# Kernel optimization log

Measured on AMD Instinct MI355X. Metric: run time of the kernel, lower is better.

## Reference

```python
import jax, jax.numpy as jnp
import numpy as np

C = 128
EPS = 1e-5


def _ln(x, g, b):
    m = jnp.mean(x, axis=-1, keepdims=True)
    v = jnp.mean((x - m) ** 2, axis=-1, keepdims=True)
    return (x - m) * jax.lax.rsqrt(v + EPS) * g + b


def setup_inputs() -> dict:
    key = jax.random.key(0)
    ks = jax.random.split(key, 10)
    B, N = 1, 384
    s = 1.0 / np.sqrt(C)
    inp = {
        "z": jax.random.normal(ks[0], (B, N, N, C), dtype=jnp.float32),
        "ln1_g": jnp.ones((C,), jnp.float32),
        "ln1_b": jnp.zeros((C,), jnp.float32),
        "ln2_g": jnp.ones((C,), jnp.float32),
        "ln2_b": jnp.zeros((C,), jnp.float32),
        "Wa": jax.random.uniform(ks[1], (C, C), jnp.float32, -s, s),
        "ba": jnp.zeros((C,), jnp.float32),
        "Wga": jax.random.uniform(ks[2], (C, C), jnp.float32, -s, s),
        "bga": jnp.zeros((C,), jnp.float32),
        "Wb": jax.random.uniform(ks[3], (C, C), jnp.float32, -s, s),
        "bb": jnp.zeros((C,), jnp.float32),
        "Wgb": jax.random.uniform(ks[4], (C, C), jnp.float32, -s, s),
        "bgb": jnp.zeros((C,), jnp.float32),
        "Wg": jax.random.uniform(ks[5], (C, C), jnp.float32, -s, s),
        "bg": jnp.zeros((C,), jnp.float32),
        "Wo": jax.random.uniform(ks[6], (C, C), jnp.float32, -s, s),
        "bo": jnp.zeros((C,), jnp.float32),
    }
    return inp


def reference(z, ln1_g, ln1_b, ln2_g, ln2_b, Wa, ba, Wga, bga, Wb, bb, Wgb, bgb, Wg, bg, Wo, bo):
    # z: (B, i, j, c)
    zn = _ln(z, ln1_g, ln1_b)
    a = (zn @ Wa + ba) * jax.nn.sigmoid(zn @ Wga + bga)      # (B,i,k,c)
    b = (zn @ Wb + bb) * jax.nn.sigmoid(zn @ Wgb + bgb)      # (B,j,k,c)
    gate = jax.nn.sigmoid(zn @ Wg + bg)                      # (B,i,j,c)
    o = jnp.einsum('bikc,bjkc->bijc', a, b)                  # outgoing triangle update
    return gate * (_ln(o, ln2_g, ln2_b) @ Wo + bo)
```

## Files before the change

### kernel.cpp

```cpp
#include <hip/hip_runtime.h>
#include <stdint.h>

typedef _Float16 f16x8 __attribute__((ext_vector_type(8)));
typedef float floatx4 __attribute__((ext_vector_type(4)));

#define RR 147456
#define NC 128
#define NN 384

union U32B { unsigned int u; _Float16 h[2]; };

__device__ inline floatx4 zero4() { floatx4 v; v[0]=0.f; v[1]=0.f; v[2]=0.f; v[3]=0.f; return v; }
__device__ inline float sigmoidf_(float x) { return 1.f / (1.f + __expf(-x)); }

__global__ __launch_bounds__(256) void k0_wt(
    const float* __restrict__ w0, const float* __restrict__ w1,
    const float* __restrict__ w2, const float* __restrict__ w3,
    const float* __restrict__ w4, const float* __restrict__ w5,
    _Float16* __restrict__ wt)
{
  const float* w;
  switch (blockIdx.x) {
    case 0: w = w0; break; case 1: w = w1; break; case 2: w = w2; break;
    case 3: w = w3; break; case 4: w = w4; break; default: w = w5; break;
  }
  _Float16* out = wt + blockIdx.x * 16384;
  const int t = threadIdx.x;
  for (int it = 0; it < 64; ++it) {
    int f = it * 256 + t;
    int n = f >> 7, k = f & 127;
    out[f] = (_Float16)w[k * 128 + n];
  }
}

__global__ __launch_bounds__(256) void k2_ln_gemm(
    const float* __restrict__ z, const float* __restrict__ ln1g, const float* __restrict__ ln1b,
    const _Float16* __restrict__ wt,
    const float* __restrict__ ba, const float* __restrict__ bga,
    const float* __restrict__ bb, const float* __restrict__ bgb,
    const float* __restrict__ bg,
    _Float16* __restrict__ at, _Float16* __restrict__ bt, _Float16* __restrict__ gate)
{
  __shared__ __align__(16) _Float16 zns[64][136];
  __shared__ __align__(16) _Float16 wts[128][136];
  const int t = threadIdx.x;
  const int w = t >> 6, lane = t & 63;
  const int l15 = lane & 15, quad = lane >> 4;
  const int r0 = blockIdx.x * 64;

  {
    float gg0 = ln1g[2*lane], gg1 = ln1g[2*lane+1];
    float bb0 = ln1b[2*lane], bb1 = ln1b[2*lane+1];
    for (int rr = 0; rr < 16; ++rr) {
      int row = w * 16 + rr;
      float2 xz = *(const float2*)(z + (size_t)(r0 + row) * NC + 2*lane);
      float x0 = xz.x, x1 = xz.y;
      float s = x0 + x1, q = x0*x0 + x1*x1;
      #pragma unroll
      for (int m = 1; m < 64; m <<= 1) { s += __shfl_xor(s, m); q += __shfl_xor(q, m); }
      float mean = s * (1.f/128.f);
      float var  = q * (1.f/128.f) - mean*mean;
      float rs = rsqrtf(var + 1e-5f);
      U32B uo;
      uo.h[0] = (_Float16)((x0 - mean) * rs * gg0 + bb0);
      uo.h[1] = (_Float16)((x1 - mean) * rs * gg1 + bb1);
      *(unsigned int*)&zns[row][2*lane] = uo.u;
    }
  }
  __syncthreads();

  auto stage = [&](const _Float16* wsrc) {
    #pragma unroll
    for (int it = 0; it < 8; ++it) {
      int f = (it * 256 + t) * 8;
      int n = f >> 7, k = f & 127;
      *(uint4*)&wts[n][k] = *(const uint4*)(wsrc + f);
    }
  };
  auto gemm = [&](floatx4* acc) {
    #pragma unroll
    for (int nt = 0; nt < 8; ++nt) acc[nt] = zero4();
    #pragma unroll
    for (int k0 = 0; k0 < 128; k0 += 32) {
      f16x8 af = *(const f16x8*)&zns[w*16 + l15][k0 + quad*8];
      #pragma unroll
      for (int nt = 0; nt < 8; ++nt) {
        f16x8 bfr = *(const f16x8*)&wts[nt*16 + l15][k0 + quad*8];
        acc[nt] = __builtin_amdgcn_mfma_f32_16x16x32_f16(af, bfr, acc[nt], 0, 0, 0);
      }
    }
  };
  auto combine_store = [&](const floatx4* aP, const floatx4* aG,
                           const float* bia, const float* big, _Float16* dst) {
    #pragma unroll
    for (int nt = 0; nt < 8; ++nt) {
      int c = nt*16 + l15;
      float bav = bia[c], bgv = big[c];
      union { uint2 u2; _Float16 h[4]; } pk;
      #pragma unroll
      for (int r = 0; r < 4; ++r) {
        float p  = aP[nt][r] + bav;
        float gg = aG[nt][r] + bgv;
        pk.h[r] = (_Float16)(p * sigmoidf_(gg));
      }
      *(uint2*)(dst + (size_t)c * RR + r0 + w*16 + quad*4) = pk.u2;
    }
  };

  floatx4 accP[8], accG[8];

  stage(wt + 0*16384); __syncthreads(); gemm(accP); __syncthreads();
  stage(wt + 1*16384); __syncthreads(); gemm(accG); __syncthreads();
  combine_store(accP, accG, ba, bga, at);
  stage(wt + 2*16384); __syncthreads(); gemm(accP); __syncthreads();
  stage(wt + 3*16384); __syncthreads(); gemm(accG); __syncthreads();
  combine_store(accP, accG, bb, bgb, bt);
  stage(wt + 4*16384); __syncthreads(); gemm(accG); __syncthreads();

  #pragma unroll
  for (int nt = 0; nt < 8; ++nt) {
    int c = nt*16 + l15;
    float bgv = bg[c];
    #pragma unroll
    for (int r = 0; r < 4; ++r)
      zns[w*16 + quad*4 + r][c] = (_Float16)sigmoidf_(accG[nt][r] + bgv);
  }
  __syncthreads();
  {
    int row = t >> 2, c0 = (t & 3) * 32;
    uint4* dst = (uint4*)(gate + (size_t)(r0 + row) * NC + c0);
    const uint4* src = (const uint4*)&zns[row][c0];
    dst[0] = src[0]; dst[1] = src[1]; dst[2] = src[2]; dst[3] = src[3];
  }
}

__global__ __launch_bounds__(256) void k3_tri(
    const _Float16* __restrict__ at, const _Float16* __restrict__ bt, float* __restrict__ o)
{
  __shared__ __align__(16) _Float16 As[128][72];
  __shared__ __align__(16) _Float16 Bs[128][72];
  const int t = threadIdx.x;
  const int w = t >> 6, lane = t & 63, l15 = lane & 15, quad = lane >> 4;
  const int c = blockIdx.y;
  const int i0 = (blockIdx.x / 3) * 128, j0 = (blockIdx.x % 3) * 128;
  const int wi = w >> 1, wj = w & 1;
  const size_t base = (size_t)c * RR;
  const _Float16* A  = at + base;
  const _Float16* Bp = bt + base;

  floatx4 acc[4][4];
  #pragma unroll
  for (int mt = 0; mt < 4; ++mt)
    #pragma unroll
    for (int nt = 0; nt < 4; ++nt) acc[mt][nt] = zero4();

  for (int kk = 0; kk < NN; kk += 64) {
    #pragma unroll
    for (int s2 = 0; s2 < 4; ++s2) {
      int f = s2 * 2048 + t * 8;
      int row = f >> 6, k = f & 63;
      *(uint4*)&As[row][k] = *(const uint4*)(A  + (size_t)(i0 + row) * NN + kk + k);
      *(uint4*)&Bs[row][k] = *(const uint4*)(Bp + (size_t)(j0 + row) * NN + kk + k);
    }
    __syncthreads();
    #pragma unroll
    for (int k0 = 0; k0 < 64; k0 += 32) {
      f16x8 af[4], bfr[4];
      #pragma unroll
      for (int mt = 0; mt < 4; ++mt) af[mt]  = *(const f16x8*)&As[wi*64 + mt*16 + l15][k0 + quad*8];
      #pragma unroll
      for (int nt = 0; nt < 4; ++nt) bfr[nt] = *(const f16x8*)&Bs[wj*64 + nt*16 + l15][k0 + quad*8];
      #pragma unroll
      for (int mt = 0; mt < 4; ++mt)
        #pragma unroll
        for (int nt = 0; nt < 4; ++nt)
          acc[mt][nt] = __builtin_amdgcn_mfma_f32_16x16x32_f16(af[mt], bfr[nt], acc[mt][nt], 0, 0, 0);
    }
    __syncthreads();
  }
  #pragma unroll
  for (int mt = 0; mt < 4; ++mt) {
    #pragma unroll
    for (int r = 0; r < 4; ++r) {
      int i = i0 + wi*64 + mt*16 + quad*4 + r;
      float* orow = o + base + (size_t)i * NN + j0 + wj*64;
      #pragma unroll
      for (int nt = 0; nt < 4; ++nt) orow[nt*16 + l15] = acc[mt][nt][r];
    }
  }
}

__global__ __launch_bounds__(256) void k4_out(
    const float* __restrict__ o, const _Float16* __restrict__ gate,
    const float* __restrict__ ln2g, const float* __restrict__ ln2b,
    const _Float16* __restrict__ wot, const float* __restrict__ bo,
    float* __restrict__ out)
{
  __shared__ __align__(16) float    osb[64][129];
  __shared__ __align__(16) _Float16 ans[64][136];
  __shared__ __align__(16) _Float16 wts[128][136];
  __shared__ __align__(16) _Float16 gbf[64][136];
  const int t = threadIdx.x;
  const int w = t >> 6, lane = t & 63, l15 = lane & 15, quad = lane >> 4;
  const int r0 = blockIdx.x * 64;

  #pragma unroll
  for (int it = 0; it < 8; ++it) {
    int f = it * 1024 + t * 4;
    int cx = f >> 6, p = f & 63;
    float4 v = *(const float4*)(o + (size_t)cx * RR + r0 + p);
    osb[p+0][cx] = v.x; osb[p+1][cx] = v.y; osb[p+2][cx] = v.z; osb[p+3][cx] = v.w;
  }
  {
    int row = t >> 2, c0 = (t & 3) * 32;
    const uint4* src = (const uint4*)(gate + (size_t)(r0 + row) * NC + c0);
    uint4* dst = (uint4*)&gbf[row][c0];
    dst[0] = src[0]; dst[1] = src[1]; dst[2] = src[2]; dst[3] = src[3];
  }
  #pragma unroll
  for (int it = 0; it < 8; ++it) {
    int f = (it * 256 + t) * 8;
    int n = f >> 7, k = f & 127;
    *(uint4*)&wts[n][k] = *(const uint4*)(wot + f);
  }
  __syncthreads();

  {
    float gg0 = ln2g[2*lane], gg1 = ln2g[2*lane+1];
    float bb0 = ln2b[2*lane], bb1 = ln2b[2*lane+1];
    for (int rr = 0; rr < 16; ++rr) {
      int row = w * 16 + rr;
      float x0 = osb[row][2*lane], x1 = osb[row][2*lane+1];
      float s = x0 + x1, q = x0*x0 + x1*x1;
      #pragma unroll
      for (int m = 1; m < 64; m <<= 1) { s += __shfl_xor(s, m); q += __shfl_xor(q, m); }
      float mean = s * (1.f/128.f);
      float var  = q * (1.f/128.f) - mean*mean;
      float rs = rsqrtf(var + 1e-5f);
      U32B uo;
      uo.h[0] = (_Float16)((x0 - mean) * rs * gg0 + bb0);
      uo.h[1] = (_Float16)((x1 - mean) * rs * gg1 + bb1);
      *(unsigned int*)&ans[row][2*lane] = uo.u;
    }
  }
  __syncthreads();

  floatx4 acc[8];
  #pragma unroll
  for (int nt = 0; nt < 8; ++nt) acc[nt] = zero4();
  #pragma unroll
  for (int k0 = 0; k0 < 128; k0 += 32) {
    f16x8 af = *(const f16x8*)&ans[w*16 + l15][k0 + quad*8];
    #pragma unroll
    for (int nt = 0; nt < 8; ++nt) {
      f16x8 bfr = *(const f16x8*)&wts[nt*16 + l15][k0 + quad*8];
      acc[nt] = __builtin_amdgcn_mfma_f32_16x16x32_f16(af, bfr, acc[nt], 0, 0, 0);
    }
  }

  #pragma unroll
  for (int nt = 0; nt < 8; ++nt) {
    int c = nt*16 + l15;
    float bov = bo[c];
    #pragma unroll
    for (int r = 0; r < 4; ++r) {
      int rl = w*16 + quad*4 + r;
      out[(size_t)(r0 + rl) * NC + c] = (float)gbf[rl][c] * (acc[nt][r] + bov);
    }
  }
}

extern "C" void kernel_launch(void* const* d_in, const int* in_sizes, int n_in,
                              void* d_out, int out_size, void* d_ws, size_t ws_size,
                              hipStream_t stream) {
  const float* z    = (const float*)d_in[0];
  const float* l1g  = (const float*)d_in[1];
  const float* l1b  = (const float*)d_in[2];
  const float* l2g  = (const float*)d_in[3];
  const float* l2b  = (const float*)d_in[4];
  const float* Wa   = (const float*)d_in[5];
  const float* ba   = (const float*)d_in[6];
  const float* Wga  = (const float*)d_in[7];
  const float* bga  = (const float*)d_in[8];
  const float* Wb   = (const float*)d_in[9];
  const float* bb   = (const float*)d_in[10];
  const float* Wgb  = (const float*)d_in[11];
  const float* bgb  = (const float*)d_in[12];
  const float* Wg   = (const float*)d_in[13];
  const float* bg   = (const float*)d_in[14];
  const float* Wo   = (const float*)d_in[15];
  const float* bo   = (const float*)d_in[16];

  char* ws = (char*)d_ws;
  _Float16* at_  = (_Float16*)(ws + 0);
  _Float16* bt_  = (_Float16*)(ws + 37748736);
  _Float16* gate = (_Float16*)(ws + 75497472);
  float*    o    = (float*)   (ws + 113246208);
  _Float16* wt   = (_Float16*)(ws + 188743680);

  hipLaunchKernelGGL(k0_wt, dim3(6), dim3(256), 0, stream, Wa, Wga, Wb, Wgb, Wg, Wo, wt);
  hipLaunchKernelGGL(k2_ln_gemm, dim3(2304), dim3(256), 0, stream,
                     z, l1g, l1b, wt, ba, bga, bb, bgb, bg, at_, bt_, gate);
  hipLaunchKernelGGL(k3_tri, dim3(9, 128), dim3(256), 0, stream, at_, bt_, o);
  hipLaunchKernelGGL(k4_out, dim3(2304), dim3(256), 0, stream,
                     o, gate, l2g, l2b, wt + 5*16384, bo, (float*)d_out);
}
```

Measured before the change: 339.4 us.

## Pre-swizzle weights into MFMA fragment order and load B operands directly from global

The weight-prep kernel now writes each weight matrix in MFMA B-fragment order, so the GEMM kernels read B fragments straight from global/L2 memory with coalesced 16-byte loads. This removes the shared-memory weight staging and its many barriers. The A fragments are hoisted into registers once. LayerNorm now uses 16 lanes per row with float4 loads and fewer shuffles. The gate tensor is stored channel-major to match the output fragment layout, which removes the shared-memory round trip in both kernels. The trade-off is repeated global/L2 reads of the weights by every wave, and strided 8-byte gate accesses.

```diff
diff --git a/kernel.cpp b/kernel.cpp
--- a/kernel.cpp
+++ b/kernel.cpp
@@ -7,8 +7,6 @@
 #define RR 147456
 #define NC 128
 #define NN 384
-
-union U32B { unsigned int u; _Float16 h[2]; };
 
 __device__ inline floatx4 zero4() { floatx4 v; v[0]=0.f; v[1]=0.f; v[2]=0.f; v[3]=0.f; return v; }
 __device__ inline float sigmoidf_(float x) { return 1.f / (1.f + __expf(-x)); }
@@ -17,76 +15,90 @@
     const float* __restrict__ w0, const float* __restrict__ w1,
     const float* __restrict__ w2, const float* __restrict__ w3,
     const float* __restrict__ w4, const float* __restrict__ w5,
-    _Float16* __restrict__ wt)
+    _Float16* __restrict__ wf)
 {
   const float* w;
   switch (blockIdx.x) {
     case 0: w = w0; break; case 1: w = w1; break; case 2: w = w2; break;
     case 3: w = w3; break; case 4: w = w4; break; default: w = w5; break;
   }
-  _Float16* out = wt + blockIdx.x * 16384;
+  _Float16* out = wf + blockIdx.x * 16384;
   const int t = threadIdx.x;
   for (int it = 0; it < 64; ++it) {
     int f = it * 256 + t;
-    int n = f >> 7, k = f & 127;
+    int j  = f & 7;
+    int ln = (f >> 3) & 63;
+    int nt = (f >> 9) & 7;
+    int k0 = f >> 12;
+    int k = k0 * 32 + (ln >> 4) * 8 + j;
+    int n = nt * 16 + (ln & 15);
     out[f] = (_Float16)w[k * 128 + n];
   }
 }
 
 __global__ __launch_bounds__(256) void k2_ln_gemm(
     const float* __restrict__ z, const float* __restrict__ ln1g, const float* __restrict__ ln1b,
-    const _Float16* __restrict__ wt,
+    const _Float16* __restrict__ wf,
     const float* __restrict__ ba, const float* __restrict__ bga,
     const float* __restrict__ bb, const float* __restrict__ bgb,
     const float* __restrict__ bg,
     _Float16* __restrict__ at, _Float16* __restrict__ bt, _Float16* __restrict__ gate)
 {
   __shared__ __align__(16) _Float16 zns[64][136];
-  __shared__ __align__(16) _Float16 wts[128][136];
   const int t = threadIdx.x;
   const int w = t >> 6, lane = t & 63;
   const int l15 = lane & 15, quad = lane >> 4;
   const int r0 = blockIdx.x * 64;
 
   {
-    float gg0 = ln1g[2*lane], gg1 = ln1g[2*lane+1];
-    float bb0 = ln1b[2*lane], bb1 = ln1b[2*lane+1];
-    for (int rr = 0; rr < 16; ++rr) {
-      int row = w * 16 + rr;
-      float2 xz = *(const float2*)(z + (size_t)(r0 + row) * NC + 2*lane);
-      float x0 = xz.x, x1 = xz.y;
-      float s = x0 + x1, q = x0*x0 + x1*x1;
-      #pragma unroll
-      for (int m = 1; m < 64; m <<= 1) { s += __shfl_xor(s, m); q += __shfl_xor(q, m); }
+    const int g = lane >> 4, h = lane & 15;
+    float4 ga = *(const float4*)(ln1g + h*8);
+    float4 gb = *(const float4*)(ln1g + h*8 + 4);
+    float4 bba = *(const float4*)(ln1b + h*8);
+    float4 bbb = *(const float4*)(ln1b + h*8 + 4);
+    #pragma unroll
+    for (int rr = 0; rr < 4; ++rr) {
+      int row = w * 16 + rr * 4 + g;
+      const float* zp = z + (size_t)(r0 + row) * NC + h * 8;
+      float4 xa = *(const float4*)zp;
+      float4 xb = *(const float4*)(zp + 4);
+      float s = xa.x + xa.y + xa.z + xa.w + xb.x + xb.y + xb.z + xb.w;
+      float q = xa.x*xa.x + xa.y*xa.y + xa.z*xa.z + xa.w*xa.w
+              + xb.x*xb.x + xb.y*xb.y + xb.z*xb.z + xb.w*xb.w;
+      #pragma unroll
+      for (int m = 1; m < 16; m <<= 1) { s += __shfl_xor(s, m); q += __shfl_xor(q, m); }
       float mean = s * (1.f/128.f);
       float var  = q * (1.f/128.f) - mean*mean;
       float rs = rsqrtf(var + 1e-5f);
-      U32B uo;
-      uo.h[0] = (_Float16)((x0 - mean) * rs * gg0 + bb0);
-      uo.h[1] = (_Float16)((x1 - mean) * rs * gg1 + bb1);
-      *(unsigned int*)&zns[row][2*lane] = uo.u;
+      union { uint4 u; _Float16 hh[8]; } pk;
+      pk.hh[0] = (_Float16)((xa.x - mean) * rs * ga.x + bba.x);
+      pk.hh[1] = (_Float16)((xa.y - mean) * rs * ga.y + bba.y);
+      pk.hh[2] = (_Float16)((xa.z - mean) * rs * ga.z + bba.z);
+      pk.hh[3] = (_Float16)((xa.w - mean) * rs * ga.w + bba.w);
+      pk.hh[4] = (_Float16)((xb.x - mean) * rs * gb.x + bbb.x);
+      pk.hh[5] = (_Float16)((xb.y - mean) * rs * gb.y + bbb.y);
+      pk.hh[6] = (_Float16)((xb.z - mean) * rs * gb.z + bbb.z);
+      pk.hh[7] = (_Float16)((xb.w - mean) * rs * gb.w + bbb.w);
+      *(uint4*)&zns[row][h * 8] = pk.u;
     }
   }
   __syncthreads();
 
-  auto stage = [&](const _Float16* wsrc) {
-    #pragma unroll
-    for (int it = 0; it < 8; ++it) {
-      int f = (it * 256 + t) * 8;
-      int n = f >> 7, k = f & 127;
-      *(uint4*)&wts[n][k] = *(const uint4*)(wsrc + f);
-    }
-  };
-  auto gemm = [&](floatx4* acc) {
+  f16x8 af[4];
+  #pragma unroll
+  for (int k0 = 0; k0 < 4; ++k0)
+    af[k0] = *(const f16x8*)&zns[w*16 + l15][k0*32 + quad*8];
+
+  auto gemm = [&](int slot, floatx4* acc) {
+    const _Float16* p = wf + slot * 16384 + lane * 8;
     #pragma unroll
     for (int nt = 0; nt < 8; ++nt) acc[nt] = zero4();
     #pragma unroll
-    for (int k0 = 0; k0 < 128; k0 += 32) {
-      f16x8 af = *(const f16x8*)&zns[w*16 + l15][k0 + quad*8];
+    for (int k0 = 0; k0 < 4; ++k0) {
       #pragma unroll
       for (int nt = 0; nt < 8; ++nt) {
-        f16x8 bfr = *(const f16x8*)&wts[nt*16 + l15][k0 + quad*8];
-        acc[nt] = __builtin_amdgcn_mfma_f32_16x16x32_f16(af, bfr, acc[nt], 0, 0, 0);
+        f16x8 bfr = *(const f16x8*)(p + (k0*8 + nt) * 512);
+        acc[nt] = __builtin_amdgcn_mfma_f32_16x16x32_f16(af[k0], bfr, acc[nt], 0, 0, 0);
       }
     }
   };
@@ -109,28 +121,18 @@
 
   floatx4 accP[8], accG[8];
 
-  stage(wt + 0*16384); __syncthreads(); gemm(accP); __syncthreads();
-  stage(wt + 1*16384); __syncthreads(); gemm(accG); __syncthreads();
-  combine_store(accP, accG, ba, bga, at);
-  stage(wt + 2*16384); __syncthreads(); gemm(accP); __syncthreads();
-  stage(wt + 3*16384); __syncthreads(); gemm(accG); __syncthreads();
-  combine_store(accP, accG, bb, bgb, bt);
-  stage(wt + 4*16384); __syncthreads(); gemm(accG); __syncthreads();
-
+  gemm(0, accP); gemm(1, accG); combine_store(accP, accG, ba, bga, at);
+  gemm(2, accP); gemm(3, accG); combine_store(accP, accG, bb, bgb, bt);
+  gemm(4, accG);
   #pragma unroll
   for (int nt = 0; nt < 8; ++nt) {
     int c = nt*16 + l15;
     float bgv = bg[c];
+    union { uint2 u2; _Float16 h[4]; } pk;
     #pragma unroll
     for (int r = 0; r < 4; ++r)
-      zns[w*16 + quad*4 + r][c] = (_Float16)sigmoidf_(accG[nt][r] + bgv);
-  }
-  __syncthreads();
-  {
-    int row = t >> 2, c0 = (t & 3) * 32;
-    uint4* dst = (uint4*)(gate + (size_t)(r0 + row) * NC + c0);
-    const uint4* src = (const uint4*)&zns[row][c0];
-    dst[0] = src[0]; dst[1] = src[1]; dst[2] = src[2]; dst[3] = src[3];
+      pk.h[r] = (_Float16)sigmoidf_(accG[nt][r] + bgv);
+    *(uint2*)(gate + (size_t)c * RR + r0 + w*16 + quad*4) = pk.u2;
   }
 }
 
@@ -193,13 +195,11 @@
 __global__ __launch_bounds__(256) void k4_out(
     const float* __restrict__ o, const _Float16* __restrict__ gate,
     const float* __restrict__ ln2g, const float* __restrict__ ln2b,
-    const _Float16* __restrict__ wot, const float* __restrict__ bo,
+    const _Float16* __restrict__ wo5, const float* __restrict__ bo,
     float* __restrict__ out)
 {
-  __shared__ __align__(16) float    osb[64][129];
+  __shared__ __align__(16) float    osb[64][132];
   __shared__ __align__(16) _Float16 ans[64][136];
-  __shared__ __align__(16) _Float16 wts[128][136];
-  __shared__ __align__(16) _Float16 gbf[64][136];
   const int t = threadIdx.x;
   const int w = t >> 6, lane = t & 63, l15 = lane & 15, quad = lane >> 4;
   const int r0 = blockIdx.x * 64;
@@ -211,50 +211,58 @@
     float4 v = *(const float4*)(o + (size_t)cx * RR + r0 + p);
     osb[p+0][cx] = v.x; osb[p+1][cx] = v.y; osb[p+2][cx] = v.z; osb[p+3][cx] = v.w;
   }
+  __syncthreads();
+
   {
-    int row = t >> 2, c0 = (t & 3) * 32;
-    const uint4* src = (const uint4*)(gate + (size_t)(r0 + row) * NC + c0);
-    uint4* dst = (uint4*)&gbf[row][c0];
-    dst[0] = src[0]; dst[1] = src[1]; dst[2] = src[2]; dst[3] = src[3];
-  }
-  #pragma unroll
-  for (int it = 0; it < 8; ++it) {
-    int f = (it * 256 + t) * 8;
-    int n = f >> 7, k = f & 127;
-    *(uint4*)&wts[n][k] = *(const uint4*)(wot + f);
-  }
-  __syncthreads();
-
-  {
-    float gg0 = ln2g[2*lane], gg1 = ln2g[2*lane+1];
-    float bb0 = ln2b[2*lane], bb1 = ln2b[2*lane+1];
-    for (int rr = 0; rr < 16; ++rr) {
-      int row = w * 16 + rr;
-      float x0 = osb[row][2*lane], x1 = osb[row][2*lane+1];
-      float s = x0 + x1, q = x0*x0 + x1*x1;
-      #pragma unroll
-      for (int m = 1; m < 64; m <<= 1) { s += __shfl_xor(s, m); q += __shfl_xor(q, m); }
+    const int g = lane >> 4, h = lane & 15;
+    float4 ga = *(const float4*)(ln2g + h*8);
+    float4 gb = *(const float4*)(ln2g + h*8 + 4);
+    float4 bba = *(const float4*)(ln2b + h*8);
+    float4 bbb = *(const float4*)(ln2b + h*8 + 4);
+    #pragma unroll
+    for (int rr = 0; rr < 4; ++rr) {
+      int row = w * 16 + rr * 4 + g;
+      float4 xa = *(const float4*)&osb[row][h*8];
+      float4 xb = *(const float4*)&osb[row][h*8 + 4];
+      float s = xa.x + xa.y + xa.z + xa.w + xb.x + xb.y + xb.z + xb.w;
+      float q = xa.x*xa.x + xa.y*xa.y + xa.z*xa.z + xa.w*xa.w
+              + xb.x*xb.x + xb.y*xb.y + xb.z*xb.z + xb.w*xb.w;
+      #pragma unroll
+      for (int m = 1; m < 16; m <<= 1) { s += __shfl_xor(s, m); q += __shfl_xor(q, m); }
       float mean = s * (1.f/128.f);
       float var  = q * (1.f/128.f) - mean*mean;
       float rs = rsqrtf(var + 1e-5f);
-      U32B uo;
-      uo.h[0] = (_Float16)((x0 - mean) * rs * gg0 + bb0);
-      uo.h[1] = (_Float16)((x1 - mean) * rs * gg1 + bb1);
-      *(unsigned int*)&ans[row][2*lane] = uo.u;
+      union { uint4 u; _Float16 hh[8]; } pk;
+      pk.hh[0] = (_Float16)((xa.x - mean) * rs * ga.x + bba.x);
+      pk.hh[1] = (_Float16)((xa.y - mean) * rs * ga.y + bba.y);
+      pk.hh[2] = (_Float16)((xa.z - mean) * rs * ga.z + bba.z);
+      pk.hh[3] = (_Float16)((xa.w - mean) * rs * ga.w + bba.w);
+      pk.hh[4] = (_Float16)((xb.x - mean) * rs * gb.x + bbb.x);
+      pk.hh[5] = (_Float16)((xb.y - mean) * rs * gb.y + bbb.y);
+      pk.hh[6] = (_Float16)((xb.z - mean) * rs * gb.z + bbb.z);
+      pk.hh[7] = (_Float16)((xb.w - mean) * rs * gb.w + bbb.w);
+      *(uint4*)&ans[row][h * 8] = pk.u;
     }
   }
   __syncthreads();
 
+  f16x8 af[4];
+  #pragma unroll
+  for (int k0 = 0; k0 < 4; ++k0)
+    af[k0] = *(const f16x8*)&ans[w*16 + l15][k0*32 + quad*8];
+
   floatx4 acc[8];
   #pragma unroll
   for (int nt = 0; nt < 8; ++nt) acc[nt] = zero4();
-  #pragma unroll
-  for (int k0 = 0; k0 < 128; k0 += 32) {
-    f16x8 af = *(const f16x8*)&ans[w*16 + l15][k0 + quad*8];
-    #pragma unroll
-    for (int nt = 0; nt < 8; ++nt) {
-      f16x8 bfr = *(const f16x8*)&wts[nt*16 + l15][k0 + quad*8];
-      acc[nt] = __builtin_amdgcn_mfma_f32_16x16x32_f16(af, bfr, acc[nt], 0, 0, 0);
+  {
+    const _Float16* p = wo5 + lane * 8;
+    #pragma unroll
+    for (int k0 = 0; k0 < 4; ++k0) {
+      #pragma unroll
+      for (int nt = 0; nt < 8; ++nt) {
+        f16x8 bfr = *(const f16x8*)(p + (k0*8 + nt) * 512);
+        acc[nt] = __builtin_amdgcn_mfma_f32_16x16x32_f16(af[k0], bfr, acc[nt], 0, 0, 0);
+      }
     }
   }
 
@@ -262,10 +270,12 @@
   for (int nt = 0; nt < 8; ++nt) {
     int c = nt*16 + l15;
     float bov = bo[c];
+    union { uint2 u2; _Float16 h[4]; } gk;
+    gk.u2 = *(const uint2*)(gate + (size_t)c * RR + r0 + w*16 + quad*4);
     #pragma unroll
     for (int r = 0; r < 4; ++r) {
       int rl = w*16 + quad*4 + r;
-      out[(size_t)(r0 + rl) * NC + c] = (float)gbf[rl][c] * (acc[nt][r] + bov);
+      out[(size_t)(r0 + rl) * NC + c] = (float)gk.h[r] * (acc[nt][r] + bov);
     }
   }
 }
@@ -296,12 +306,12 @@
   _Float16* bt_  = (_Float16*)(ws + 37748736);
   _Float16* gate = (_Float16*)(ws + 75497472);
   float*    o    = (float*)   (ws + 113246208);
-  _Float16* wt   = (_Float16*)(ws + 188743680);
-
-  hipLaunchKernelGGL(k0_wt, dim3(6), dim3(256), 0, stream, Wa, Wga, Wb, Wgb, Wg, Wo, wt);
+  _Float16* wf   = (_Float16*)(ws + 188743680);
+
+  hipLaunchKernelGGL(k0_wt, dim3(6), dim3(256), 0, stream, Wa, Wga, Wb, Wgb, Wg, Wo, wf);
   hipLaunchKernelGGL(k2_ln_gemm, dim3(2304), dim3(256), 0, stream,
-                     z, l1g, l1b, wt, ba, bga, bb, bgb, bg, at_, bt_, gate);
+                     z, l1g, l1b, wf, ba, bga, bb, bgb, bg, at_, bt_, gate);
   hipLaunchKernelGGL(k3_tri, dim3(9, 128), dim3(256), 0, stream, at_, bt_, o);
   hipLaunchKernelGGL(k4_out, dim3(2304), dim3(256), 0, stream,
-                     o, gate, l2g, l2b, wt + 5*16384, bo, (float*)d_out);
-}
+                     o, gate, l2g, l2b, wf + 5*16384, bo, (float*)d_out);
+}
```

Result: slower. 391.4 us (+15.3%).
